# Performance work log

Hardware: AMD Instinct MI355X
Metric: run time of the kernel (lower is better)

## Reference

```python
import jax, jax.numpy as jnp
import numpy as np

DIM = 1024
HEADS = 16
HEAD_DIM = DIM // HEADS
MLP_HIDDEN = 4 * DIM
OUT_DIM = 1000
V_DIM = 1024
EPS = 1e-5
SCALE = DIM ** -0.5  # note: module scales by hidden_dim**-0.5, not head_dim**-0.5


def layer_norm(x, g, b):
    mu = jnp.mean(x, axis=-1, keepdims=True)
    var = jnp.mean(jnp.square(x - mu), axis=-1, keepdims=True)
    return (x - mu) * jax.lax.rsqrt(var + EPS) * g + b


def setup_inputs() -> dict:
    key = jax.random.key(0)
    ks = jax.random.split(key, 12)
    B, N = 4, 2048
    s = lambda fan_in: 1.0 / np.sqrt(fan_in)
    return {
        "x": jax.random.normal(ks[0], (B, N, DIM), jnp.float32),
        "value": jax.random.normal(ks[1], (B, N, V_DIM), jnp.float32),
        "wq": jax.random.normal(ks[2], (DIM, DIM), jnp.float32) * s(DIM),
        "wk": jax.random.normal(ks[3], (DIM, DIM), jnp.float32) * s(DIM),
        "wv": jax.random.normal(ks[4], (V_DIM, DIM), jnp.float32) * s(V_DIM),
        "w_ap": jax.random.normal(ks[5], (DIM, DIM), jnp.float32) * s(DIM),
        "b_ap": jnp.zeros((DIM,), jnp.float32),
        "g1": jnp.ones((DIM,), jnp.float32),
        "be1": jnp.zeros((DIM,), jnp.float32),
        "g2": jnp.ones((DIM,), jnp.float32),
        "be2": jnp.zeros((DIM,), jnp.float32),
        "w1": jax.random.normal(ks[6], (DIM, MLP_HIDDEN), jnp.float32) * s(DIM),
        "b1": jnp.zeros((MLP_HIDDEN,), jnp.float32),
        "w2": jax.random.normal(ks[7], (MLP_HIDDEN, DIM), jnp.float32) * s(MLP_HIDDEN),
        "b2": jnp.zeros((DIM,), jnp.float32),
        "w_out": jax.random.normal(ks[8], (DIM, OUT_DIM), jnp.float32) * s(DIM),
        "b_out": jnp.zeros((OUT_DIM,), jnp.float32),
    }


def reference(x, value, wq, wk, wv, w_ap, b_ap, g1, be1, g2, be2, w1, b1, w2, b2, w_out, b_out):
    B, N, C = x.shape
    xn = layer_norm(x, g1, be1)                      # [B,N,C]
    q = (xn @ wq).reshape(B, N, HEADS, HEAD_DIM)     # query and key both from norm1(x)
    k = (xn @ wk).reshape(B, N, HEADS, HEAD_DIM)
    v = (value @ wv).reshape(B, N, HEADS, HEAD_DIM)
    attn = jnp.einsum("bqhd,bkhd->bhqk", q, k) * SCALE
    attn = jax.nn.softmax(attn, axis=-1)
    o = jnp.einsum("bhqk,bkhd->bqhd", attn, v).reshape(B, N, C)
    x = x + (o @ w_ap + b_ap)                        # residual (dropouts are identity)
    h = jax.nn.gelu(layer_norm(x, g2, be2) @ w1 + b1, approximate=False)
    x = x + (h @ w2 + b2)
    return jax.nn.softmax(x @ w_out + b_out, axis=2)
```

## Files before the change

### kernel.cpp

```cpp
#include <hip/hip_runtime.h>
#include <math.h>

typedef unsigned short u16;
typedef unsigned int u32;
typedef __attribute__((ext_vector_type(4))) float f32x4;
typedef __attribute__((ext_vector_type(4))) int i32x4;
typedef __attribute__((ext_vector_type(8))) short short8;
typedef __attribute__((ext_vector_type(4))) unsigned short u16x4;
typedef __attribute__((ext_vector_type(4))) __fp16 f16x4;
typedef __attribute__((ext_vector_type(2))) __fp16 f16x2;

#define DEV __device__ __forceinline__

DEV u16 f2bf(float f) {
  unsigned u = __float_as_uint(f);
  u += 0x7FFFu + ((u >> 16) & 1u);
  return (u16)(u >> 16);
}

DEV float fexp2(float x) {
  float r;
  asm("v_exp_f32 %0, %1" : "=v"(r) : "v"(x));
  return r;
}

DEV void gload_lds16(const void* g, void* l) {
  __builtin_amdgcn_global_load_lds((const __attribute__((address_space(1))) void*)g,
                                   (__attribute__((address_space(3))) void*)l, 16, 0, 0);
}

template<int N> DEV void waitv() {
  if constexpr (N == 4)      asm volatile("s_waitcnt vmcnt(4)" ::: "memory");
  else if constexpr (N == 3) asm volatile("s_waitcnt vmcnt(3)" ::: "memory");
  else if constexpr (N == 2) asm volatile("s_waitcnt vmcnt(2)" ::: "memory");
  else                       asm volatile("s_waitcnt vmcnt(0)" ::: "memory");
}

DEV void bar() {
  asm volatile("s_barrier" ::: "memory");
}

enum { EPI_QK = 0, EPI_VT = 1, EPI_RESID_F32 = 2, EPI_GELU = 3, EPI_RESID_BF16 = 4, EPI_LOGITS = 5 };

__global__ void transpose_w(const float* __restrict__ in, u16* __restrict__ out,
                            int K, int Nsrc, int Nout) {
  __shared__ float tile[32][33];
  int k0 = blockIdx.x * 32, n0 = blockIdx.y * 32;
  int tx = threadIdx.x, ty = threadIdx.y;
#pragma unroll
  for (int i = 0; i < 4; ++i) {
    int k = k0 + ty + i * 8, n = n0 + tx;
    tile[ty + i * 8][tx] = (n < Nsrc) ? in[(size_t)k * Nsrc + n] : 0.0f;
  }
  __syncthreads();
#pragma unroll
  for (int i = 0; i < 4; ++i) {
    int n = n0 + ty + i * 8, k = k0 + tx;
    out[(size_t)n * K + k] = f2bf(tile[tx][ty + i * 8]);
  }
}

__global__ void convert_bf16(const float* __restrict__ in, u16* __restrict__ out, int n4) {
  int i = blockIdx.x * blockDim.x + threadIdx.x;
  int stride = gridDim.x * blockDim.x;
  for (int j = i; j < n4; j += stride) {
    f32x4 v = reinterpret_cast<const f32x4*>(in)[j];
    u16x4 o;
    o[0] = f2bf(v[0]); o[1] = f2bf(v[1]); o[2] = f2bf(v[2]); o[3] = f2bf(v[3]);
    reinterpret_cast<u16x4*>(out)[j] = o;
  }
}

DEV float blockReduceSum(float v) {
  __shared__ float red[4];
#pragma unroll
  for (int m = 32; m >= 1; m >>= 1) v += __shfl_xor(v, m);
  __syncthreads();
  if ((threadIdx.x & 63) == 0) red[threadIdx.x >> 6] = v;
  __syncthreads();
  return red[0] + red[1] + red[2] + red[3];
}

DEV float blockReduceMax(float v) {
  __shared__ float redm[4];
#pragma unroll
  for (int m = 32; m >= 1; m >>= 1) v = fmaxf(v, __shfl_xor(v, m));
  __syncthreads();
  if ((threadIdx.x & 63) == 0) redm[threadIdx.x >> 6] = v;
  __syncthreads();
  return fmaxf(fmaxf(redm[0], redm[1]), fmaxf(redm[2], redm[3]));
}

__global__ __launch_bounds__(256)
void layernorm_k(const float* __restrict__ x, const float* __restrict__ g,
                 const float* __restrict__ b, u16* __restrict__ out) {
  int row = blockIdx.x, t = threadIdx.x;
  const float* xr = x + (size_t)row * 1024;
  f32x4 v = *reinterpret_cast<const f32x4*>(xr + t * 4);
  float mu = blockReduceSum(v[0] + v[1] + v[2] + v[3]) * (1.0f / 1024.0f);
  f32x4 d;
  d[0] = v[0] - mu; d[1] = v[1] - mu; d[2] = v[2] - mu; d[3] = v[3] - mu;
  float var = blockReduceSum(d[0]*d[0] + d[1]*d[1] + d[2]*d[2] + d[3]*d[3]) * (1.0f / 1024.0f);
  float rstd = rsqrtf(var + 1e-5f);
  u16x4 o;
#pragma unroll
  for (int i = 0; i < 4; ++i) o[i] = f2bf(d[i] * rstd * g[t * 4 + i] + b[t * 4 + i]);
  *reinterpret_cast<u16x4*>(out + (size_t)row * 1024 + t * 4) = o;
}

__global__ __launch_bounds__(256)
void softmax_rows(float* __restrict__ io) {
  int row = blockIdx.x, t = threadIdx.x;
  float* p = io + (size_t)row * 1000;
  float v[4];
  float mx = -INFINITY;
#pragma unroll
  for (int i = 0; i < 4; ++i) {
    int c = t + i * 256;
    v[i] = (c < 1000) ? p[c] : -INFINITY;
    mx = fmaxf(mx, v[i]);
  }
  mx = blockReduceMax(mx);
  float s = 0.f;
#pragma unroll
  for (int i = 0; i < 4; ++i) {
    int c = t + i * 256;
    v[i] = (c < 1000) ? __expf(v[i] - mx) : 0.f;
    s += v[i];
  }
  s = blockReduceSum(s);
  float inv = 1.0f / s;
#pragma unroll
  for (int i = 0; i < 4; ++i) {
    int c = t + i * 256;
    if (c < 1000) p[c] = v[i] * inv;
  }
}

template<int EPI, int BN>
__global__ __launch_bounds__(512, 1)
void gemm_8ph(const u16* __restrict__ A, const u16* __restrict__ Bt,
              void* __restrict__ outp, const float* __restrict__ aux0,
              const float* __restrict__ aux1, int M, int N, int K, float scale) {
  constexpr int NJ = BN / 64;
  __shared__ u16 As[2][256 * 64];
  __shared__ u16 Bs[2][BN * 64];

  const int t = threadIdx.x;
  const int lane = t & 63;
  const int w = t >> 6;
  const int wm = w >> 2, wn = w & 3;
  const int bm = blockIdx.y * 256, bn = blockIdx.x * BN;
  const int l15 = lane & 15, lg = lane >> 4;
  const int nt = K >> 6;

  f32x4 acc[8][NJ] = {};
  short8 aR[4][2], bR[2][2];

  auto stA = [&](int buf, int kt, int q) {
    int rl = q * 64 + (t >> 3), s0 = t & 7;
    gload_lds16(A + (size_t)(bm + rl) * K + kt * 64 + (s0 ^ (rl & 7)) * 8,
                &As[buf][q * 4096 + t * 8]);
  };
  auto stB = [&](int buf, int kt, int q) {
    int rl = q * 64 + (t >> 3), s0 = t & 7;
    gload_lds16(Bt + (size_t)(bn + rl) * K + kt * 64 + (s0 ^ (rl & 7)) * 8,
                &Bs[buf][q * 4096 + t * 8]);
  };
  auto rdA = [&](int buf, int mh) {
#pragma unroll
    for (int i2 = 0; i2 < 4; ++i2) {
      int rA = wm * 128 + mh * 64 + i2 * 16 + l15;
#pragma unroll
      for (int ks = 0; ks < 2; ++ks)
        aR[i2][ks] = *reinterpret_cast<const short8*>(
            &As[buf][rA * 64 + (((ks * 4 + lg) ^ (rA & 7)) * 8)]);
    }
  };
  auto rdB = [&](int buf, int nh) {
#pragma unroll
    for (int j2 = 0; j2 < 2; ++j2) {
      int rB = (BN == 256) ? (wn * 64 + nh * 32 + j2 * 16 + l15)
                           : (wn * 32 + j2 * 16 + l15);
#pragma unroll
      for (int ks = 0; ks < 2; ++ks)
        bR[j2][ks] = *reinterpret_cast<const short8*>(
            &Bs[buf][rB * 64 + (((ks * 4 + lg) ^ (rB & 7)) * 8)]);
    }
  };
  auto domfma = [&](int mh, int nh) {
    __builtin_amdgcn_s_setprio(1);
#pragma unroll
    for (int i2 = 0; i2 < 4; ++i2)
#pragma unroll
      for (int j2 = 0; j2 < 2; ++j2)
#pragma unroll
        for (int ks = 0; ks < 2; ++ks)
          acc[mh * 4 + i2][nh * 2 + j2] = __builtin_amdgcn_mfma_f32_16x16x32_bf16(
              aR[i2][ks], bR[j2][ks], acc[mh * 4 + i2][nh * 2 + j2], 0, 0, 0);
    __builtin_amdgcn_s_setprio(0);
  };

  if constexpr (BN == 256) {
    stB(0, 0, 0); stB(0, 0, 1); stB(0, 0, 2); stB(0, 0, 3);
    stA(0, 0, 0); stA(0, 0, 2); stA(0, 0, 1); stA(0, 0, 3);
  } else {
    stB(0, 0, 0); stB(0, 0, 1);
    stA(0, 0, 0); stA(0, 0, 2); stA(0, 0, 1); stA(0, 0, 3);
  }

#pragma unroll 1
  for (int tt = 0; tt < nt; ++tt) {
    const int buf = tt & 1, nb = buf ^ 1;
    const bool pf = (tt + 1 < nt);
    if constexpr (BN == 256) {
      waitv<2>();
      bar();
      rdA(buf, 0); rdB(buf, 0);
      if (pf) { stB(nb, tt + 1, 0); stB(nb, tt + 1, 1); }
      domfma(0, 0);
      bar();
      rdB(buf, 1);
      if (pf) { stB(nb, tt + 1, 2); stB(nb, tt + 1, 3); }
      domfma(0, 1);
      if (pf) waitv<4>(); else waitv<0>();
      bar();
      rdA(buf, 1);
      if (pf) { stA(nb, tt + 1, 0); stA(nb, tt + 1, 2); }
      domfma(1, 1);
      bar();
      rdB(buf, 0);
      if (pf) { stA(nb, tt + 1, 1); stA(nb, tt + 1, 3); }
      domfma(1, 0);
    } else {
      waitv<2>();
      bar();
      rdA(buf, 0); rdB(buf, 0);
      if (pf) { stB(nb, tt + 1, 0); stB(nb, tt + 1, 1); stA(nb, tt + 1, 0); }
      domfma(0, 0);
      if (pf) waitv<3>(); else waitv<0>();
      bar();
      rdA(buf, 1);
      if (pf) { stA(nb, tt + 1, 2); stA(nb, tt + 1, 1); stA(nb, tt + 1, 3); }
      domfma(1, 0);
    }
  }

#pragma unroll
  for (int i = 0; i < 8; ++i)
#pragma unroll
    for (int j = 0; j < NJ; ++j)
#pragma unroll
      for (int r = 0; r < 4; ++r) {
        int row = bm + wm * 128 + i * 16 + lg * 4 + r;
        int col = bn + wn * (BN / 4) + j * 16 + l15;
        float v = acc[i][j][r];
        if constexpr (EPI == EPI_QK) {
          float sc = (col < 1024) ? 0.03125f * 1.44269504088896f : 1.0f;
          ((u16*)outp)[(size_t)row * 2048 + col] = f2bf(v * sc);
        } else if constexpr (EPI == EPI_VT) {
          size_t idx = ((size_t)((row >> 11) * 16 + (col >> 6)) * 64 + (col & 63)) * 2048 + (row & 2047);
          __fp16 hv = (__fp16)v;
          ((u16*)outp)[idx] = *reinterpret_cast<u16*>(&hv);
        } else if constexpr (EPI == EPI_RESID_F32) {
          ((float*)outp)[(size_t)row * N + col] = v + aux0[col] + aux1[(size_t)row * N + col];
        } else if constexpr (EPI == EPI_GELU) {
          float tt2 = v + aux0[col];
          float u = tt2 * (0.7978845608f + 0.035677408f * tt2 * tt2);
          float e = fexp2(u * 2.8853900818f);
          float gl = tt2 * (1.0f - 1.0f / (1.0f + e));
          ((u16*)outp)[(size_t)row * N + col] = f2bf(gl);
        } else if constexpr (EPI == EPI_RESID_BF16) {
          float tt2 = v + aux0[col] + aux1[(size_t)row * N + col];
          ((u16*)outp)[(size_t)row * N + col] = f2bf(tt2);
        } else {
          if (col < 1000) ((float*)outp)[(size_t)row * 1000 + col] = v + aux0[col];
        }
      }
  (void)scale; (void)aux0; (void)aux1; (void)M;
}

__global__ __launch_bounds__(512)
void attn_flash(const u16* __restrict__ QKb, const u16* __restrict__ Vt,
                u16* __restrict__ Ob) {
  __shared__ u16 Ks[2][128 * 64];
  __shared__ u16 Vs[2][64 * 128];
  const int t = threadIdx.x;
  const int lane = t & 63, w = t >> 6;
  const int l15 = lane & 15, lg = lane >> 4;
  const int bh = blockIdx.x;
  const int b = bh >> 4, h = bh & 15;
  const int qrow0 = b * 2048 + blockIdx.y * 128 + w * 16;

  short8 qf[2];
#pragma unroll
  for (int ks = 0; ks < 2; ++ks)
    qf[ks] = *reinterpret_cast<const short8*>(QKb + (size_t)(qrow0 + l15) * 2048 + h * 64 + ks * 32 + lg * 8);

  f32x4 oacc[4] = {};
  float lpart = 0.f;

  const int sgK = ((t & 7) ^ ((t >> 3) & 7)) * 8;
  const int sgV = ((t & 15) ^ ((t >> 4) & 7)) * 8;
  const int tk8 = t * 8;

  auto STAGE = [&](int buf, int tt) {
    int kt = tt * 128;
#pragma unroll
    for (int p = 0; p < 2; ++p) {
      int rK = p * 64 + (t >> 3);
      gload_lds16(QKb + (size_t)(b * 2048 + kt + rK) * 2048 + 1024 + h * 64 + sgK, &Ks[buf][p * 4096 + tk8]);
      int rV = p * 32 + (t >> 4);
      gload_lds16(Vt + ((size_t)bh * 64 + rV) * 2048 + kt + sgV, &Vs[buf][p * 4096 + tk8]);
    }
  };

  auto COMPUTE = [&](int buf) {
    f32x4 s[8];
#pragma unroll
    for (int cb = 0; cb < 8; ++cb) {
      s[cb] = f32x4{0.f, 0.f, 0.f, 0.f};
      int rK = cb * 16 + l15;
#pragma unroll
      for (int ks = 0; ks < 2; ++ks) {
        int sk = (lg + ks * 4) ^ (rK & 7);
        short8 kf = *reinterpret_cast<const short8*>(&Ks[buf][rK * 64 + sk * 8]);
        s[cb] = __builtin_amdgcn_mfma_f32_16x16x32_bf16(kf, qf[ks], s[cb], 0, 0, 0);
      }
    }

    const char* vbase = (const char*)&Vs[buf][0];
#pragma unroll
    for (int cb = 0; cb < 8; ++cb) {
      float e0 = fexp2(s[cb][0]), e1 = fexp2(s[cb][1]);
      float e2 = fexp2(s[cb][2]), e3 = fexp2(s[cb][3]);
      lpart += (e0 + e1) + (e2 + e3);
      f16x2 plo = __builtin_amdgcn_cvt_pkrtz(e0, e1);
      f16x2 phi = __builtin_amdgcn_cvt_pkrtz(e2, e3);
      f16x4 pf;
      pf[0] = plo[0]; pf[1] = plo[1]; pf[2] = phi[0]; pf[3] = phi[1];
#pragma unroll
      for (int db = 0; db < 4; ++db) {
        int d = db * 16 + l15;
        int boff = d * 256 + ((((2 * cb + (lg >> 1)) ^ (d & 7)) << 4) | ((lg & 1) << 3));
        f16x4 vf = *reinterpret_cast<const f16x4*>(vbase + boff);
        oacc[db] = __builtin_amdgcn_mfma_f32_16x16x16f16(pf, vf, oacc[db], 0, 0, 0);
      }
    }
  };

  STAGE(0, 0);
  __syncthreads();
#pragma unroll 1
  for (int i = 0; i < 8; ++i) {
    STAGE(1, 2 * i + 1);
    COMPUTE(0);
    __syncthreads();
    if (i < 7) STAGE(0, 2 * i + 2);
    COMPUTE(1);
    __syncthreads();
  }

  lpart += __shfl_xor(lpart, 16);
  lpart += __shfl_xor(lpart, 32);
  float inv = 1.0f / lpart;
  float invr[4];
#pragma unroll
  for (int r = 0; r < 4; ++r) invr[r] = __shfl(inv, lg * 4 + r);

#pragma unroll
  for (int db = 0; db < 4; ++db)
#pragma unroll
    for (int r = 0; r < 4; ++r) {
      int row = qrow0 + lg * 4 + r;
      int col = h * 64 + db * 16 + l15;
      Ob[(size_t)row * 1024 + col] = f2bf(oacc[db][r] * invr[r]);
    }
}

extern "C" void kernel_launch(void* const* d_in, const int* in_sizes, int n_in,
                              void* d_out, int out_size, void* d_ws, size_t ws_size,
                              hipStream_t stream) {
  (void)in_sizes; (void)n_in; (void)out_size; (void)ws_size;
  const float* x     = (const float*)d_in[0];
  const float* value = (const float*)d_in[1];
  const float* wq    = (const float*)d_in[2];
  const float* wk    = (const float*)d_in[3];
  const float* wv    = (const float*)d_in[4];
  const float* w_ap  = (const float*)d_in[5];
  const float* b_ap  = (const float*)d_in[6];
  const float* g1    = (const float*)d_in[7];
  const float* be1   = (const float*)d_in[8];
  const float* g2    = (const float*)d_in[9];
  const float* be2   = (const float*)d_in[10];
  const float* w1    = (const float*)d_in[11];
  const float* b1    = (const float*)d_in[12];
  const float* w2    = (const float*)d_in[13];
  const float* b2    = (const float*)d_in[14];
  const float* w_out = (const float*)d_in[15];
  const float* b_out = (const float*)d_in[16];

  char* ws = (char*)d_ws;
  u16* wqT   = (u16*)(ws + 0x0000000);
  u16* wkT   = (u16*)(ws + 0x0200000);
  u16* wvT   = (u16*)(ws + 0x0400000);
  u16* wapT  = (u16*)(ws + 0x0600000);
  u16* woutT = (u16*)(ws + 0x0800000);
  u16* w1T   = (u16*)(ws + 0x0A00000);
  u16* w2T   = (u16*)(ws + 0x1200000);
  u16* xn    = (u16*)(ws + 0x1A00000);
  u16* valb  = (u16*)(ws + 0x2A00000);
  u16* qkb   = (u16*)(ws + 0x3A00000);
  u16* vT    = (u16*)(ws + 0x5A00000);
  u16* ob    = (u16*)(ws + 0x6A00000);
  float* x1  = (float*)(ws + 0x7A00000);
  u16* hb    = valb;
  u16* xn2   = xn;
  u16* x2b   = ob;

  dim3 tb(32, 8);
  transpose_w<<<dim3(32, 32),  tb, 0, stream>>>(wq,    wqT,   1024, 1024, 1024);
  transpose_w<<<dim3(32, 32),  tb, 0, stream>>>(wk,    wkT,   1024, 1024, 1024);
  transpose_w<<<dim3(32, 32),  tb, 0, stream>>>(wv,    wvT,   1024, 1024, 1024);
  transpose_w<<<dim3(32, 32),  tb, 0, stream>>>(w_ap,  wapT,  1024, 1024, 1024);
  transpose_w<<<dim3(32, 32),  tb, 0, stream>>>(w_out, woutT, 1024, 1000, 1024);
  transpose_w<<<dim3(32, 128), tb, 0, stream>>>(w1,    w1T,   1024, 4096, 4096);
  transpose_w<<<dim3(128, 32), tb, 0, stream>>>(w2,    w2T,   4096, 1024, 1024);

  convert_bf16<<<2048, 256, 0, stream>>>(value, valb, 2097152);
  layernorm_k<<<8192, 256, 0, stream>>>(x, g1, be1, xn);

  gemm_8ph<EPI_QK, 256><<<dim3(8, 32),  512, 0, stream>>>(xn,   wqT, qkb, nullptr, nullptr, 8192, 2048, 1024, 1.0f);
  gemm_8ph<EPI_VT, 128><<<dim3(8, 32),  512, 0, stream>>>(valb, wvT, vT,  nullptr, nullptr, 8192, 1024, 1024, 1.0f);

  attn_flash<<<dim3(64, 16), 512, 0, stream>>>(qkb, vT, ob);

  gemm_8ph<EPI_RESID_F32, 128><<<dim3(8, 32),  512, 0, stream>>>(ob,  wapT, x1, b_ap, x, 8192, 1024, 1024, 1.0f);
  layernorm_k<<<8192, 256, 0, stream>>>(x1, g2, be2, xn2);
  gemm_8ph<EPI_GELU, 256>     <<<dim3(16, 32), 512, 0, stream>>>(xn2, w1T, hb, b1, nullptr, 8192, 4096, 1024, 1.0f);
  gemm_8ph<EPI_RESID_BF16, 128><<<dim3(8, 32), 512, 0, stream>>>(hb,  w2T, x2b, b2, x1, 8192, 1024, 4096, 1.0f);
  gemm_8ph<EPI_LOGITS, 128>   <<<dim3(8, 32),  512, 0, stream>>>(x2b, woutT, (float*)d_out, b_out, nullptr, 8192, 1024, 1024, 1.0f);
  softmax_rows<<<8192, 256, 0, stream>>>((float*)d_out);
}
```

Before: 453.7 us.

## Store residual x1 in bf16, remap GEMM blocks across XCDs, prioritize attention MFMA

The post-attention residual x1 is now stored as bf16 instead of fp32. A new bf16 layernorm reads it, and the w2 epilogue reads it as bf16, which cuts the bytes moved for that intermediate. GEMM workgroup indices are remapped so consecutive tiles land on the same XCD, aiming for better L2 reuse. The attention kernel raises wave priority around MFMA sections with s_setprio. Storing the residual in bf16 loses precision on the residual stream.

```diff
diff --git a/kernel.cpp b/kernel.cpp
--- a/kernel.cpp
+++ b/kernel.cpp
@@ -18,6 +18,8 @@
   return (u16)(u >> 16);
 }
 
+DEV float bf2f(u16 b) { return __uint_as_float(((u32)b) << 16); }
+
 DEV float fexp2(float x) {
   float r;
   asm("v_exp_f32 %0, %1" : "=v"(r) : "v"(x));
@@ -40,7 +42,7 @@
   asm volatile("s_barrier" ::: "memory");
 }
 
-enum { EPI_QK = 0, EPI_VT = 1, EPI_RESID_F32 = 2, EPI_GELU = 3, EPI_RESID_BF16 = 4, EPI_LOGITS = 5 };
+enum { EPI_QK = 0, EPI_VT = 1, EPI_RESID_X1 = 2, EPI_GELU = 3, EPI_RESID_BF16 = 4, EPI_LOGITS = 5 };
 
 __global__ void transpose_w(const float* __restrict__ in, u16* __restrict__ out,
                             int K, int Nsrc, int Nout) {
@@ -109,6 +111,26 @@
 }
 
 __global__ __launch_bounds__(256)
+void layernorm_bf16(const u16* __restrict__ x, const float* __restrict__ g,
+                    const float* __restrict__ b, u16* __restrict__ out) {
+  int row = blockIdx.x, t = threadIdx.x;
+  const u16* xr = x + (size_t)row * 1024;
+  u16x4 raw = *reinterpret_cast<const u16x4*>(xr + t * 4);
+  f32x4 v;
+#pragma unroll
+  for (int i = 0; i < 4; ++i) v[i] = bf2f(raw[i]);
+  float mu = blockReduceSum(v[0] + v[1] + v[2] + v[3]) * (1.0f / 1024.0f);
+  f32x4 d;
+  d[0] = v[0] - mu; d[1] = v[1] - mu; d[2] = v[2] - mu; d[3] = v[3] - mu;
+  float var = blockReduceSum(d[0]*d[0] + d[1]*d[1] + d[2]*d[2] + d[3]*d[3]) * (1.0f / 1024.0f);
+  float rstd = rsqrtf(var + 1e-5f);
+  u16x4 o;
+#pragma unroll
+  for (int i = 0; i < 4; ++i) o[i] = f2bf(d[i] * rstd * g[t * 4 + i] + b[t * 4 + i]);
+  *reinterpret_cast<u16x4*>(out + (size_t)row * 1024 + t * 4) = o;
+}
+
+__global__ __launch_bounds__(256)
 void softmax_rows(float* __restrict__ io) {
   int row = blockIdx.x, t = threadIdx.x;
   float* p = io + (size_t)row * 1000;
@@ -150,7 +172,10 @@
   const int lane = t & 63;
   const int w = t >> 6;
   const int wm = w >> 2, wn = w & 3;
-  const int bm = blockIdx.y * 256, bn = blockIdx.x * BN;
+  const int flat = blockIdx.y * gridDim.x + blockIdx.x;
+  const int qch = (gridDim.x * gridDim.y) >> 3;
+  const int nid = (flat & 7) * qch + (flat >> 3);
+  const int bm = (nid / gridDim.x) * 256, bn = (nid % gridDim.x) * BN;
   const int l15 = lane & 15, lg = lane >> 4;
   const int nt = K >> 6;
 
@@ -262,8 +287,8 @@
           size_t idx = ((size_t)((row >> 11) * 16 + (col >> 6)) * 64 + (col & 63)) * 2048 + (row & 2047);
           __fp16 hv = (__fp16)v;
           ((u16*)outp)[idx] = *reinterpret_cast<u16*>(&hv);
-        } else if constexpr (EPI == EPI_RESID_F32) {
-          ((float*)outp)[(size_t)row * N + col] = v + aux0[col] + aux1[(size_t)row * N + col];
+        } else if constexpr (EPI == EPI_RESID_X1) {
+          ((u16*)outp)[(size_t)row * N + col] = f2bf(v + aux0[col] + aux1[(size_t)row * N + col]);
         } else if constexpr (EPI == EPI_GELU) {
           float tt2 = v + aux0[col];
           float u = tt2 * (0.7978845608f + 0.035677408f * tt2 * tt2);
@@ -271,8 +296,8 @@
           float gl = tt2 * (1.0f - 1.0f / (1.0f + e));
           ((u16*)outp)[(size_t)row * N + col] = f2bf(gl);
         } else if constexpr (EPI == EPI_RESID_BF16) {
-          float tt2 = v + aux0[col] + aux1[(size_t)row * N + col];
-          ((u16*)outp)[(size_t)row * N + col] = f2bf(tt2);
+          float res = bf2f(((const u16*)aux1)[(size_t)row * N + col]);
+          ((u16*)outp)[(size_t)row * N + col] = f2bf(v + aux0[col] + res);
         } else {
           if (col < 1000) ((float*)outp)[(size_t)row * 1000 + col] = v + aux0[col];
         }
@@ -317,6 +342,7 @@
 
   auto COMPUTE = [&](int buf) {
     f32x4 s[8];
+    __builtin_amdgcn_s_setprio(1);
 #pragma unroll
     for (int cb = 0; cb < 8; ++cb) {
       s[cb] = f32x4{0.f, 0.f, 0.f, 0.f};
@@ -328,6 +354,7 @@
         s[cb] = __builtin_amdgcn_mfma_f32_16x16x32_bf16(kf, qf[ks], s[cb], 0, 0, 0);
       }
     }
+    __builtin_amdgcn_s_setprio(0);
 
     const char* vbase = (const char*)&Vs[buf][0];
 #pragma unroll
@@ -339,6 +366,7 @@
       f16x2 phi = __builtin_amdgcn_cvt_pkrtz(e2, e3);
       f16x4 pf;
       pf[0] = plo[0]; pf[1] = plo[1]; pf[2] = phi[0]; pf[3] = phi[1];
+      __builtin_amdgcn_s_setprio(1);
 #pragma unroll
       for (int db = 0; db < 4; ++db) {
         int d = db * 16 + l15;
@@ -346,6 +374,7 @@
         f16x4 vf = *reinterpret_cast<const f16x4*>(vbase + boff);
         oacc[db] = __builtin_amdgcn_mfma_f32_16x16x16f16(pf, vf, oacc[db], 0, 0, 0);
       }
+      __builtin_amdgcn_s_setprio(0);
     }
   };
 
@@ -413,7 +442,7 @@
   u16* qkb   = (u16*)(ws + 0x3A00000);
   u16* vT    = (u16*)(ws + 0x5A00000);
   u16* ob    = (u16*)(ws + 0x6A00000);
-  float* x1  = (float*)(ws + 0x7A00000);
+  u16* x1b   = (u16*)(ws + 0x7A00000);
   u16* hb    = valb;
   u16* xn2   = xn;
   u16* x2b   = ob;
@@ -435,10 +464,10 @@
 
   attn_flash<<<dim3(64, 16), 512, 0, stream>>>(qkb, vT, ob);
 
-  gemm_8ph<EPI_RESID_F32, 128><<<dim3(8, 32),  512, 0, stream>>>(ob,  wapT, x1, b_ap, x, 8192, 1024, 1024, 1.0f);
-  layernorm_k<<<8192, 256, 0, stream>>>(x1, g2, be2, xn2);
+  gemm_8ph<EPI_RESID_X1, 128><<<dim3(8, 32),  512, 0, stream>>>(ob,  wapT, x1b, b_ap, x, 8192, 1024, 1024, 1.0f);
+  layernorm_bf16<<<8192, 256, 0, stream>>>(x1b, g2, be2, xn2);
   gemm_8ph<EPI_GELU, 256>     <<<dim3(16, 32), 512, 0, stream>>>(xn2, w1T, hb, b1, nullptr, 8192, 4096, 1024, 1.0f);
-  gemm_8ph<EPI_RESID_BF16, 128><<<dim3(8, 32), 512, 0, stream>>>(hb,  w2T, x2b, b2, x1, 8192, 1024, 4096, 1.0f);
+  gemm_8ph<EPI_RESID_BF16, 128><<<dim3(8, 32), 512, 0, stream>>>(hb,  w2T, x2b, b2, (const float*)x1b, 8192, 1024, 4096, 1.0f);
   gemm_8ph<EPI_LOGITS, 128>   <<<dim3(8, 32),  512, 0, stream>>>(x2b, woutT, (float*)d_out, b_out, nullptr, 8192, 1024, 1024, 1.0f);
   softmax_rows<<<8192, 256, 0, stream>>>((float*)d_out);
 }
```

New measurement: 424.5 us. 1.07x faster.
